# Optimization experiments

Measured on AMD Instinct MI355X. Metric: run time of the kernel, lower is better.

The kernel has to match this reference:

```python
import jax, jax.numpy as jnp
import numpy as np

EPS = 1e-6
NUM_HEADS = 12

def _phi(x):
    # elu(x) + 1 feature map
    return jax.nn.elu(x) + 1.0

def setup_inputs() -> dict:
    key = jax.random.key(0)
    k1, k2, k3, k4 = jax.random.split(key, 4)
    B, N, C = 4, 4096, 768
    x = jax.random.normal(k1, (B, N, C), dtype=jnp.float32)
    # nn.Linear(dim, 3*dim, bias=False): weight [3C, C]
    W_qkv = jax.random.normal(k2, (3 * C, C), dtype=jnp.float32) * (1.0 / np.sqrt(C))
    # nn.Linear(dim, dim): weight [C, C], bias [C]
    W_proj = jax.random.normal(k3, (C, C), dtype=jnp.float32) * (1.0 / np.sqrt(C))
    b_proj = jax.random.normal(k4, (C,), dtype=jnp.float32) * 0.01
    return {"x": x, "W_qkv": W_qkv, "W_proj": W_proj, "b_proj": b_proj}

def reference(x, W_qkv, W_proj, b_proj):
    B, N, C = x.shape
    H = NUM_HEADS
    d = C // H
    qkv = (x @ W_qkv.T).reshape(B, N, 3, H, d)
    qkv = jnp.transpose(qkv, (2, 0, 3, 1, 4))  # [3,B,H,N,d]
    q, k, v = qkv[0], qkv[1], qkv[2]
    q = _phi(q)
    k = _phi(k)
    # kv outer-product accumulation: [B,H,m,d] (m = value dim = d)
    kv = jnp.einsum('bhnd,bhnm->bhmd', k, v)
    # normalizer: z[b,h,n] = 1 / (q . sum_n k + eps)
    k_sum = k.sum(axis=-2)                                 # [B,H,d]
    z = 1.0 / (jnp.einsum('bhnd,bhd->bhn', q, k_sum) + EPS)
    # output: y[b,h,n,m] = sum_d q[bhnd] kv[bhmd] * z[bhn]
    y = jnp.einsum('bhnd,bhmd,bhn->bhnm', q, kv, z)        # [B,H,N,d]
    y = jnp.transpose(y, (0, 2, 1, 3)).reshape(B, N, C)
    # output projection
    return y @ W_proj.T + b_proj
```

## Files before the change

kernel.cpp:

```cpp
#include <hip/hip_runtime.h>
#include <cstdint>
#include <cstddef>


typedef __attribute__((ext_vector_type(8))) short bf16x8;
typedef __attribute__((ext_vector_type(4))) float f32x4;

__device__ __forceinline__ unsigned short f2bf(float f) {
  uint32_t u = __builtin_bit_cast(uint32_t, f);
  u += 0x7FFFu + ((u >> 16) & 1u);
  return (unsigned short)(u >> 16);
}
__device__ __forceinline__ float bf2f(unsigned short h) {
  uint32_t u = ((uint32_t)h) << 16;
  return __builtin_bit_cast(float, u);
}

__global__ __launch_bounds__(256) void cast3_kernel(
    const float* __restrict__ a, const float* __restrict__ b,
    const float* __restrict__ c, unsigned short* __restrict__ oa,
    unsigned short* __restrict__ ob, unsigned short* __restrict__ oc,
    int na4, int nb4, int nc4) {
  int i = blockIdx.x * 256 + threadIdx.x;
  const float* src;
  unsigned short* dst;
  if (i < na4) {
    src = a; dst = oa;
  } else if (i < na4 + nb4) {
    i -= na4; src = b; dst = ob;
  } else if (i < na4 + nb4 + nc4) {
    i -= na4 + nb4; src = c; dst = oc;
  } else {
    return;
  }
  float4 v = reinterpret_cast<const float4*>(src)[i];
  ushort4 o;
  o.x = f2bf(v.x); o.y = f2bf(v.y); o.z = f2bf(v.z); o.w = f2bf(v.w);
  reinterpret_cast<ushort4*>(dst)[i] = o;
}

#define GLOAD_LDS16(g, s)                                                     \
  __builtin_amdgcn_global_load_lds(                                           \
      (const __attribute__((address_space(1))) void*)(g),                     \
      (__attribute__((address_space(3))) void*)(s), 16, 0, 0)

template <int PHI_COLS, bool OUT_BF16, bool BIAS>
__global__ __launch_bounds__(256) void gemm128(
    const unsigned short* __restrict__ A, const unsigned short* __restrict__ B,
    void* __restrict__ Cout, const float* __restrict__ bias, int M, int N, int K) {
  __shared__ unsigned short As[128 * 64];
  __shared__ unsigned short Bs[128 * 64];
  const int t = threadIdx.x;
  const int w = t >> 6;
  const int l = t & 63;
  const int r16 = l & 15;
  const int c4 = l >> 4;

  const int nx = gridDim.x;
  const int nwg = gridDim.x * gridDim.y;
  int lin = blockIdx.y * nx + blockIdx.x;
  {
    const int q = nwg >> 3, r = nwg & 7;
    const int xcd = lin & 7, idx = lin >> 3;
    lin = (xcd < r ? xcd * (q + 1) : r * (q + 1) + (xcd - r) * q) + idx;
  }
  const int m0 = (lin / nx) * 128;
  const int n0 = (lin % nx) * 128;

  const int srow = t >> 3;
  const int schunk = (t & 7) ^ ((t >> 3) & 7);
  const unsigned short* gA = A + (size_t)(m0 + srow) * K + schunk * 8;
  const unsigned short* gB = B + (size_t)(n0 + srow) * K + schunk * 8;
  const int lbase = w * 512;

  const int wm = (w >> 1) * 64;
  const int wn = (w & 1) * 64;

  f32x4 acc[4][4] = {};

  for (int k0 = 0; k0 < K; k0 += 64) {
#pragma unroll
    for (int i = 0; i < 4; ++i) {
      GLOAD_LDS16(gA + k0 + (size_t)i * 32 * K, &As[lbase + i * 2048]);
      GLOAD_LDS16(gB + k0 + (size_t)i * 32 * K, &Bs[lbase + i * 2048]);
    }
    __syncthreads();
#pragma unroll
    for (int kk = 0; kk < 2; ++kk) {
      bf16x8 af[4], bfr[4];
#pragma unroll
      for (int mi = 0; mi < 4; ++mi) {
        const int R = wm + mi * 16 + r16;
        const int ch = (kk * 4 + c4) ^ (R & 7);
        af[mi] = *reinterpret_cast<const bf16x8*>(&As[R * 64 + ch * 8]);
      }
#pragma unroll
      for (int ni = 0; ni < 4; ++ni) {
        const int R = wn + ni * 16 + r16;
        const int ch = (kk * 4 + c4) ^ (R & 7);
        bfr[ni] = *reinterpret_cast<const bf16x8*>(&Bs[R * 64 + ch * 8]);
      }
#pragma unroll
      for (int mi = 0; mi < 4; ++mi)
#pragma unroll
        for (int ni = 0; ni < 4; ++ni)
          acc[mi][ni] = __builtin_amdgcn_mfma_f32_16x16x32_bf16(af[mi], bfr[ni], acc[mi][ni], 0, 0, 0);
    }
    __syncthreads();
  }

  const int rbase = c4 * 4;
#pragma unroll
  for (int mi = 0; mi < 4; ++mi) {
    const int row = m0 + wm + mi * 16 + rbase;
#pragma unroll
    for (int ni = 0; ni < 4; ++ni) {
      const int col = n0 + wn + ni * 16 + r16;
      float bv = 0.0f;
      if constexpr (BIAS) bv = bias[col];
      f32x4 v = acc[mi][ni];
#pragma unroll
      for (int r = 0; r < 4; ++r) {
        float x = v[r] + bv;
        if constexpr (PHI_COLS > 0) {
          if (col < PHI_COLS) x = (x > 0.0f) ? (x + 1.0f) : __expf(x);
        }
        if constexpr (OUT_BF16)
          ((unsigned short*)Cout)[(size_t)(row + r) * N + col] = f2bf(x);
        else
          ((float*)Cout)[(size_t)(row + r) * N + col] = x;
      }
    }
  }
}

__global__ __launch_bounds__(256) void kv_partial_kernel(
    const unsigned short* __restrict__ qkv, float* __restrict__ kv_part,
    float* __restrict__ ksum_part) {
  const int bh = blockIdx.x;
  const int chunk = blockIdx.y;
  const int b = bh / 12, h = bh % 12;
  const int t = threadIdx.x;
  const int tm = (t >> 4) * 4;
  const int td = (t & 15) * 4;
  const unsigned short* base = qkv + ((size_t)(b * 4096 + chunk * 256)) * 2304;
  const unsigned short* kptr = base + 768 + h * 64 + td;
  const unsigned short* vptr = base + 1536 + h * 64 + tm;
  float acc[4][4] = {};
  float ks[4] = {};
#pragma unroll 4
  for (int n = 0; n < 256; ++n) {
    const size_t off = (size_t)n * 2304;
    ushort4 ku = *reinterpret_cast<const ushort4*>(kptr + off);
    ushort4 vu = *reinterpret_cast<const ushort4*>(vptr + off);
    float kf[4] = {bf2f(ku.x), bf2f(ku.y), bf2f(ku.z), bf2f(ku.w)};
    float vf[4] = {bf2f(vu.x), bf2f(vu.y), bf2f(vu.z), bf2f(vu.w)};
#pragma unroll
    for (int i = 0; i < 4; ++i)
#pragma unroll
      for (int j = 0; j < 4; ++j) acc[i][j] += vf[i] * kf[j];
#pragma unroll
    for (int j = 0; j < 4; ++j) ks[j] += kf[j];
  }
  float* kvp = kv_part + ((size_t)(bh * 16 + chunk)) * 4096;
#pragma unroll
  for (int i = 0; i < 4; ++i)
#pragma unroll
    for (int j = 0; j < 4; ++j) kvp[(tm + i) * 64 + td + j] = acc[i][j];
  if (tm == 0) {
    float* ksp = ksum_part + (size_t)(bh * 16 + chunk) * 64;
#pragma unroll
    for (int j = 0; j < 4; ++j) ksp[td + j] = ks[j];
  }
}

__global__ __launch_bounds__(256) void kv_reduce_kernel(
    const float* __restrict__ kv_part, const float* __restrict__ ksum_part,
    unsigned short* __restrict__ kvb, float* __restrict__ ksum) {
  const int bh = blockIdx.x;
  const int t = threadIdx.x;
  for (int e = t; e < 4096; e += 256) {
    float s = 0.f;
#pragma unroll
    for (int c = 0; c < 16; ++c) s += kv_part[((size_t)(bh * 16 + c)) * 4096 + e];
    kvb[(size_t)bh * 4096 + e] = f2bf(s);
  }
  if (t < 64) {
    float s = 0.f;
#pragma unroll
    for (int c = 0; c < 16; ++c) s += ksum_part[(size_t)(bh * 16 + c) * 64 + t];
    ksum[bh * 64 + t] = s;
  }
}

__global__ __launch_bounds__(256) void y_mfma_kernel(
    const unsigned short* __restrict__ qkv, const unsigned short* __restrict__ kvb,
    const float* __restrict__ ksum, unsigned short* __restrict__ ybf) {
  __shared__ unsigned short Qs[128 * 64];
  __shared__ unsigned short KVs[64 * 64];
  __shared__ float zs[128];
  const int bh = blockIdx.x;
  const int n0 = blockIdx.y * 128;
  const int b = bh / 12, h = bh % 12;
  const int t = threadIdx.x;
  const int w = t >> 6;
  const int l = t & 63;
  const int r16 = l & 15;
  const int c4 = l >> 4;

  const int srow = t >> 3;
  const int schunk = (t & 7) ^ ((t >> 3) & 7);
  const unsigned short* gQ =
      qkv + ((size_t)(b * 4096 + n0 + srow)) * 2304 + h * 64 + schunk * 8;
  const unsigned short* gKV = kvb + (size_t)bh * 4096 + srow * 64 + schunk * 8;
  const int lbase = w * 512;
#pragma unroll
  for (int i = 0; i < 4; ++i)
    GLOAD_LDS16(gQ + (size_t)i * 32 * 2304, &Qs[lbase + i * 2048]);
#pragma unroll
  for (int i = 0; i < 2; ++i)
    GLOAD_LDS16(gKV + i * 32 * 64, &KVs[lbase + i * 2048]);
  __syncthreads();

  const int wr = w * 32;
  f32x4 acc[2][4] = {};
#pragma unroll
  for (int kk = 0; kk < 2; ++kk) {
    bf16x8 af[2], bfr[4];
#pragma unroll
    for (int mi = 0; mi < 2; ++mi) {
      const int R = wr + mi * 16 + r16;
      const int ch = (kk * 4 + c4) ^ (R & 7);
      af[mi] = *reinterpret_cast<const bf16x8*>(&Qs[R * 64 + ch * 8]);
    }
#pragma unroll
    for (int ni = 0; ni < 4; ++ni) {
      const int R = ni * 16 + r16;
      const int ch = (kk * 4 + c4) ^ (R & 7);
      bfr[ni] = *reinterpret_cast<const bf16x8*>(&KVs[R * 64 + ch * 8]);
    }
#pragma unroll
    for (int mi = 0; mi < 2; ++mi)
#pragma unroll
      for (int ni = 0; ni < 4; ++ni)
        acc[mi][ni] = __builtin_amdgcn_mfma_f32_16x16x32_bf16(af[mi], bfr[ni], acc[mi][ni], 0, 0, 0);
  }

  if (t < 128) {
    const float* ks = ksum + bh * 64;
    float s = 0.f;
#pragma unroll
    for (int c = 0; c < 8; ++c) {
      bf16x8 qv = *reinterpret_cast<const bf16x8*>(&Qs[t * 64 + ((c ^ (t & 7)) * 8)]);
#pragma unroll
      for (int j = 0; j < 8; ++j) s += bf2f((unsigned short)qv[j]) * ks[c * 8 + j];
    }
    zs[t] = 1.0f / (s + 1e-6f);
  }
  __syncthreads();

  unsigned short* ybase = ybf + ((size_t)(b * 4096 + n0)) * 768 + h * 64;
#pragma unroll
  for (int mi = 0; mi < 2; ++mi) {
#pragma unroll
    for (int ni = 0; ni < 4; ++ni) {
      const int col = ni * 16 + r16;
      f32x4 v = acc[mi][ni];
#pragma unroll
      for (int r = 0; r < 4; ++r) {
        const int row = wr + mi * 16 + c4 * 4 + r;
        ybase[(size_t)row * 768 + col] = f2bf(v[r] * zs[row]);
      }
    }
  }
}

extern "C" void kernel_launch(void* const* d_in, const int* in_sizes, int n_in,
                              void* d_out, int out_size, void* d_ws, size_t ws_size,
                              hipStream_t stream) {
  const float* x = (const float*)d_in[0];
  const float* Wqkv = (const float*)d_in[1];
  const float* Wproj = (const float*)d_in[2];
  const float* bproj = (const float*)d_in[3];
  float* out = (float*)d_out;

  const int M = 16384;
  const int C = 768;
  const int N1 = 2304;

  char* ws = (char*)d_ws;
  size_t off = 0;
  unsigned short* xb = (unsigned short*)(ws + off);  off += (size_t)M * C * 2;
  unsigned short* wqb = (unsigned short*)(ws + off); off += (size_t)N1 * C * 2;
  unsigned short* wpb = (unsigned short*)(ws + off); off += (size_t)C * C * 2;
  unsigned short* qkvb = (unsigned short*)(ws + off); off += (size_t)M * N1 * 2;
  unsigned short* kvb = (unsigned short*)(ws + off); off += (size_t)48 * 4096 * 2;
  float* ksum = (float*)(ws + off);      off += (size_t)48 * 64 * 4;
  unsigned short* yb = (unsigned short*)(ws + off); off += (size_t)M * C * 2;
  float* kv_part = (float*)xb;
  float* ksum_part = (float*)(xb + (size_t)48 * 16 * 4096 * 2);

  const int na4 = M * C / 4, nb4 = N1 * C / 4, nc4 = C * C / 4;
  cast3_kernel<<<(na4 + nb4 + nc4 + 255) / 256, 256, 0, stream>>>(
      x, Wqkv, Wproj, xb, wqb, wpb, na4, nb4, nc4);

  gemm128<1536, true, false>
      <<<dim3(N1 / 128, M / 128), 256, 0, stream>>>(xb, wqb, qkvb, nullptr, M, N1, C);

  kv_partial_kernel<<<dim3(48, 16), 256, 0, stream>>>(qkvb, kv_part, ksum_part);
  kv_reduce_kernel<<<48, 256, 0, stream>>>(kv_part, ksum_part, kvb, ksum);
  y_mfma_kernel<<<dim3(48, 32), 256, 0, stream>>>(qkvb, kvb, ksum, yb);

  gemm128<0, false, true>
      <<<dim3(C / 128, M / 128), 256, 0, stream>>>(yb, wpb, out, bproj, M, C, C);
}
```

Baseline: 180.9 us.

## Double-buffer GEMM LDS tiles with K=32 stages and split kv partials finer

The GEMM now uses two LDS buffers of K=32 slices with a new XOR swizzle. Each loop iteration issues the next tile's global-to-LDS loads before computing on the current tile, so memory latency overlaps with MFMA work and there are fewer barrier stalls. The kv partial accumulation moves from 16 chunks of 256 rows to 32 chunks of 128, for more parallelism at the cost of a larger reduction. ksum_part gets its own workspace region, since the doubled kv_part buffer (aliased onto xb) would otherwise overlap it.

Result: slower. 195.8 us (+8.2%).

```diff
diff --git a/kernel.cpp b/kernel.cpp
--- a/kernel.cpp
+++ b/kernel.cpp
@@ -45,11 +45,13 @@
       (__attribute__((address_space(3))) void*)(s), 16, 0, 0)
 
 template <int PHI_COLS, bool OUT_BF16, bool BIAS>
-__global__ __launch_bounds__(256) void gemm128(
+__global__ __launch_bounds__(256) void gemm128_db(
     const unsigned short* __restrict__ A, const unsigned short* __restrict__ B,
     void* __restrict__ Cout, const float* __restrict__ bias, int M, int N, int K) {
-  __shared__ unsigned short As[128 * 64];
-  __shared__ unsigned short Bs[128 * 64];
+  __shared__ unsigned short As0[128 * 32];
+  __shared__ unsigned short Bs0[128 * 32];
+  __shared__ unsigned short As1[128 * 32];
+  __shared__ unsigned short Bs1[128 * 32];
   const int t = threadIdx.x;
   const int w = t >> 6;
   const int l = t & 63;
@@ -67,47 +69,55 @@
   const int m0 = (lin / nx) * 128;
   const int n0 = (lin % nx) * 128;
 
-  const int srow = t >> 3;
-  const int schunk = (t & 7) ^ ((t >> 3) & 7);
-  const unsigned short* gA = A + (size_t)(m0 + srow) * K + schunk * 8;
-  const unsigned short* gB = B + (size_t)(n0 + srow) * K + schunk * 8;
-  const int lbase = w * 512;
+  const int srow = t >> 2;
+  const int csrc = (t & 3) ^ ((t >> 3) & 3);
+  const unsigned short* gA = A + (size_t)(m0 + srow) * K + csrc * 8;
+  const unsigned short* gB = B + (size_t)(n0 + srow) * K + csrc * 8;
+  const int lb = w * 512;
 
   const int wm = (w >> 1) * 64;
   const int wn = (w & 1) * 64;
+  const int rch = (c4 ^ ((r16 >> 1) & 3)) * 8;
 
   f32x4 acc[4][4] = {};
 
-  for (int k0 = 0; k0 < K; k0 += 64) {
-#pragma unroll
-    for (int i = 0; i < 4; ++i) {
-      GLOAD_LDS16(gA + k0 + (size_t)i * 32 * K, &As[lbase + i * 2048]);
-      GLOAD_LDS16(gB + k0 + (size_t)i * 32 * K, &Bs[lbase + i * 2048]);
-    }
+#define STAGE(kt_, AS_, BS_)                                                  \
+  {                                                                           \
+    const int k0_ = (kt_) * 32;                                               \
+    GLOAD_LDS16(gA + k0_, &AS_[lb]);                                          \
+    GLOAD_LDS16(gA + k0_ + (size_t)64 * K, &AS_[2048 + lb]);                  \
+    GLOAD_LDS16(gB + k0_, &BS_[lb]);                                          \
+    GLOAD_LDS16(gB + k0_ + (size_t)64 * K, &BS_[2048 + lb]);                  \
+  }
+
+#define COMP(AS_, BS_)                                                        \
+  {                                                                           \
+    bf16x8 af[4], bq[4];                                                      \
+    _Pragma("unroll") for (int mi = 0; mi < 4; ++mi)                          \
+        af[mi] = *reinterpret_cast<const bf16x8*>(                            \
+            &AS_[(wm + mi * 16 + r16) * 32 + rch]);                           \
+    _Pragma("unroll") for (int ni = 0; ni < 4; ++ni)                          \
+        bq[ni] = *reinterpret_cast<const bf16x8*>(                            \
+            &BS_[(wn + ni * 16 + r16) * 32 + rch]);                           \
+    _Pragma("unroll") for (int mi = 0; mi < 4; ++mi)                          \
+        _Pragma("unroll") for (int ni = 0; ni < 4; ++ni)                      \
+            acc[mi][ni] = __builtin_amdgcn_mfma_f32_16x16x32_bf16(            \
+                af[mi], bq[ni], acc[mi][ni], 0, 0, 0);                        \
+  }
+
+  const int ktiles = K >> 5;
+  STAGE(0, As0, Bs0)
+  __syncthreads();
+  for (int t2 = 0; t2 < ktiles; t2 += 2) {
+    if (t2 + 1 < ktiles) STAGE(t2 + 1, As1, Bs1)
+    COMP(As0, Bs0)
     __syncthreads();
-#pragma unroll
-    for (int kk = 0; kk < 2; ++kk) {
-      bf16x8 af[4], bfr[4];
-#pragma unroll
-      for (int mi = 0; mi < 4; ++mi) {
-        const int R = wm + mi * 16 + r16;
-        const int ch = (kk * 4 + c4) ^ (R & 7);
-        af[mi] = *reinterpret_cast<const bf16x8*>(&As[R * 64 + ch * 8]);
-      }
-#pragma unroll
-      for (int ni = 0; ni < 4; ++ni) {
-        const int R = wn + ni * 16 + r16;
-        const int ch = (kk * 4 + c4) ^ (R & 7);
-        bfr[ni] = *reinterpret_cast<const bf16x8*>(&Bs[R * 64 + ch * 8]);
-      }
-#pragma unroll
-      for (int mi = 0; mi < 4; ++mi)
-#pragma unroll
-        for (int ni = 0; ni < 4; ++ni)
-          acc[mi][ni] = __builtin_amdgcn_mfma_f32_16x16x32_bf16(af[mi], bfr[ni], acc[mi][ni], 0, 0, 0);
-    }
+    if (t2 + 2 < ktiles) STAGE(t2 + 2, As0, Bs0)
+    COMP(As1, Bs1)
     __syncthreads();
   }
+#undef STAGE
+#undef COMP
 
   const int rbase = c4 * 4;
 #pragma unroll
@@ -143,13 +153,13 @@
   const int t = threadIdx.x;
   const int tm = (t >> 4) * 4;
   const int td = (t & 15) * 4;
-  const unsigned short* base = qkv + ((size_t)(b * 4096 + chunk * 256)) * 2304;
+  const unsigned short* base = qkv + ((size_t)(b * 4096 + chunk * 128)) * 2304;
   const unsigned short* kptr = base + 768 + h * 64 + td;
   const unsigned short* vptr = base + 1536 + h * 64 + tm;
   float acc[4][4] = {};
   float ks[4] = {};
-#pragma unroll 4
-  for (int n = 0; n < 256; ++n) {
+#pragma unroll 8
+  for (int n = 0; n < 128; ++n) {
     const size_t off = (size_t)n * 2304;
     ushort4 ku = *reinterpret_cast<const ushort4*>(kptr + off);
     ushort4 vu = *reinterpret_cast<const ushort4*>(vptr + off);
@@ -162,13 +172,13 @@
 #pragma unroll
     for (int j = 0; j < 4; ++j) ks[j] += kf[j];
   }
-  float* kvp = kv_part + ((size_t)(bh * 16 + chunk)) * 4096;
+  float* kvp = kv_part + ((size_t)(bh * 32 + chunk)) * 4096;
 #pragma unroll
   for (int i = 0; i < 4; ++i)
 #pragma unroll
     for (int j = 0; j < 4; ++j) kvp[(tm + i) * 64 + td + j] = acc[i][j];
   if (tm == 0) {
-    float* ksp = ksum_part + (size_t)(bh * 16 + chunk) * 64;
+    float* ksp = ksum_part + (size_t)(bh * 32 + chunk) * 64;
 #pragma unroll
     for (int j = 0; j < 4; ++j) ksp[td + j] = ks[j];
   }
@@ -182,13 +192,13 @@
   for (int e = t; e < 4096; e += 256) {
     float s = 0.f;
 #pragma unroll
-    for (int c = 0; c < 16; ++c) s += kv_part[((size_t)(bh * 16 + c)) * 4096 + e];
+    for (int c = 0; c < 32; ++c) s += kv_part[((size_t)(bh * 32 + c)) * 4096 + e];
     kvb[(size_t)bh * 4096 + e] = f2bf(s);
   }
   if (t < 64) {
     float s = 0.f;
 #pragma unroll
-    for (int c = 0; c < 16; ++c) s += ksum_part[(size_t)(bh * 16 + c) * 64 + t];
+    for (int c = 0; c < 32; ++c) s += ksum_part[(size_t)(bh * 32 + c) * 64 + t];
     ksum[bh * 64 + t] = s;
   }
 }
@@ -297,20 +307,20 @@
   unsigned short* kvb = (unsigned short*)(ws + off); off += (size_t)48 * 4096 * 2;
   float* ksum = (float*)(ws + off);      off += (size_t)48 * 64 * 4;
   unsigned short* yb = (unsigned short*)(ws + off); off += (size_t)M * C * 2;
+  float* ksum_part = (float*)(ws + off); off += (size_t)48 * 32 * 64 * 4;
   float* kv_part = (float*)xb;
-  float* ksum_part = (float*)(xb + (size_t)48 * 16 * 4096 * 2);
 
   const int na4 = M * C / 4, nb4 = N1 * C / 4, nc4 = C * C / 4;
   cast3_kernel<<<(na4 + nb4 + nc4 + 255) / 256, 256, 0, stream>>>(
       x, Wqkv, Wproj, xb, wqb, wpb, na4, nb4, nc4);
 
-  gemm128<1536, true, false>
+  gemm128_db<1536, true, false>
       <<<dim3(N1 / 128, M / 128), 256, 0, stream>>>(xb, wqb, qkvb, nullptr, M, N1, C);
 
-  kv_partial_kernel<<<dim3(48, 16), 256, 0, stream>>>(qkvb, kv_part, ksum_part);
+  kv_partial_kernel<<<dim3(48, 32), 256, 0, stream>>>(qkvb, kv_part, ksum_part);
   kv_reduce_kernel<<<48, 256, 0, stream>>>(kv_part, ksum_part, kvb, ksum);
   y_mfma_kernel<<<dim3(48, 32), 256, 0, stream>>>(qkvb, kvb, ksum, yb);
 
-  gemm128<0, false, true>
+  gemm128_db<0, false, true>
       <<<dim3(C / 128, M / 128), 256, 0, stream>>>(yb, wpb, out, bproj, M, C, C);
 }
```
